# Performance work log

Hardware: AMD Instinct MI355X
Metric: run time of the kernel (lower is better)

## Reference

```python
import jax, jax.numpy as jnp
import numpy as np

GRAPH_SIZE = 1024
D_MODEL = 256
BATCH = 32
INITIAL_ALPHA = 1.0


def setup_inputs() -> dict:
    key = jax.random.key(0)
    ks = jax.random.split(key, 10)
    s = 1.0 / np.sqrt(D_MODEL)  # torch Linear default init scale
    inp = {
        "query": jax.random.normal(ks[0], (BATCH, GRAPH_SIZE, D_MODEL), jnp.float32),
        "key_": jax.random.normal(ks[1], (BATCH, GRAPH_SIZE, D_MODEL), jnp.float32),
        "value": jax.random.normal(ks[2], (BATCH, GRAPH_SIZE, D_MODEL), jnp.float32),
        "dist": jax.random.uniform(ks[3], (BATCH, GRAPH_SIZE, GRAPH_SIZE), jnp.float32),
        "Wq": jax.random.uniform(ks[4], (D_MODEL, D_MODEL), jnp.float32, -s, s),
        "bq": jax.random.uniform(ks[5], (D_MODEL,), jnp.float32, -s, s),
        "Wk": jax.random.uniform(ks[6], (D_MODEL, D_MODEL), jnp.float32, -s, s),
        "bk": jax.random.uniform(ks[7], (D_MODEL,), jnp.float32, -s, s),
        "Wv": jax.random.uniform(ks[8], (D_MODEL, D_MODEL), jnp.float32, -s, s),
        "bv": jax.random.uniform(ks[9], (D_MODEL,), jnp.float32, -s, s),
        # alpha_raw = exp(initial_alpha - 1)
        "alpha_raw": jnp.asarray(np.exp(INITIAL_ALPHA - 1.0), jnp.float32),
    }
    return inp


def reference(query, key_, value, dist, Wq, bq, Wk, bk, Wv, bv, alpha_raw):
    # self-attention path: mask=None, cross=False, query_size == graph_size
    log2_N = jnp.log2(jnp.asarray(GRAPH_SIZE, jnp.float32))
    alpha = jax.nn.softplus(alpha_raw) + 1e-6

    q = jnp.einsum('bnd,ed->bne', query, Wq) + bq   # fc_q
    k = jnp.einsum('bnd,ed->bne', key_, Wk) + bk    # fc_k
    v = jnp.einsum('bnd,ed->bne', value, Wv) + bv   # fc_v

    exp_A = jnp.exp(-alpha * log2_N * dist)         # [b, n, n]
    exp_K = jnp.exp(k)                              # [b, n, d]

    numerator = jnp.einsum('bqk,bkd->bqd', exp_A, exp_K * v)
    denominator = jnp.einsum('bqk,bkd->bqd', exp_A, exp_K) + 1e-8
    return jax.nn.sigmoid(q) * (numerator / denominator)
```

## Files before the change

### kernel.cpp

```cpp
#include <hip/hip_runtime.h>
#include <hip/hip_bf16.h>

#define NBATCH 32
#define NG 1024
#define DM 256

typedef short bf16x8 __attribute__((ext_vector_type(8)));
typedef float f32x4 __attribute__((ext_vector_type(4)));
typedef unsigned short u16x4 __attribute__((ext_vector_type(4)));
typedef unsigned short u16x8 __attribute__((ext_vector_type(8)));

static __device__ __forceinline__ unsigned short f2bf(float f) {
    __hip_bfloat16 h = __float2bfloat16(f);
    return *reinterpret_cast<unsigned short*>(&h);
}

static __device__ __forceinline__ void gload16(const void* g, void* l) {
    __builtin_amdgcn_global_load_lds(
        (const __attribute__((address_space(1))) unsigned int*)g,
        (__attribute__((address_space(3))) unsigned int*)l, 16, 0, 0);
}

static __device__ __forceinline__ void wait_vm8_bar() {
    asm volatile("s_waitcnt vmcnt(8)" ::: "memory");
    asm volatile("s_barrier" ::: "memory");
    __builtin_amdgcn_sched_barrier(0);
}
static __device__ __forceinline__ void wait_vm0_bar() {
    asm volatile("s_waitcnt vmcnt(0)" ::: "memory");
    asm volatile("s_barrier" ::: "memory");
    __builtin_amdgcn_sched_barrier(0);
}
static __device__ __forceinline__ void bar_only() {
    asm volatile("s_barrier" ::: "memory");
}

__global__ __launch_bounds__(256) void wpack_kernel(
    const float* __restrict__ Wq, const float* __restrict__ Wk,
    const float* __restrict__ Wv, unsigned short* __restrict__ Wb)
{
    const int i4 = (blockIdx.x * 256 + threadIdx.x) * 4;
    const int t = i4 >> 16;
    const int off = i4 & 65535;
    const float* src = (t == 0) ? Wq : (t == 1) ? Wk : Wv;
    float4 v = *(const float4*)(src + off);
    *(u16x4*)(Wb + i4) = (u16x4){ f2bf(v.x), f2bf(v.y), f2bf(v.z), f2bf(v.w) };
}

__global__ __launch_bounds__(256) void conv3_kernel(
    const float* __restrict__ q, const float* __restrict__ k,
    const float* __restrict__ v, unsigned short* __restrict__ Xb)
{
    const int sel = blockIdx.x >> 12;
    const float* src = (sel == 0) ? q : (sel == 1) ? k : v;
    const size_t i8 = (((size_t)(blockIdx.x & 4095)) * 256 + threadIdx.x) * 8;
    float4 a = *(const float4*)(src + i8);
    float4 b = *(const float4*)(src + i8 + 4);
    *(u16x8*)(Xb + (size_t)sel * NBATCH * NG * DM + i8) =
        (u16x8){ f2bf(a.x), f2bf(a.y), f2bf(a.z), f2bf(a.w),
                 f2bf(b.x), f2bf(b.y), f2bf(b.z), f2bf(b.w) };
}

__global__ __launch_bounds__(256) void exp_kernel(
    const float* __restrict__ dist, unsigned short* __restrict__ ea,
    const float* __restrict__ alpha_raw)
{
    const float alpha = log1pf(__expf(alpha_raw[0])) + 1e-6f;
    const float sc = -alpha * 10.0f * 1.44269504088896f;
    const size_t i8 = ((size_t)blockIdx.x * 256 + threadIdx.x) * 8;
    float4 v0 = *(const float4*)(dist + i8);
    float4 v1 = *(const float4*)(dist + i8 + 4);
    u16x8 o = { f2bf(exp2f(sc * v0.x)), f2bf(exp2f(sc * v0.y)),
                f2bf(exp2f(sc * v0.z)), f2bf(exp2f(sc * v0.w)),
                f2bf(exp2f(sc * v1.x)), f2bf(exp2f(sc * v1.y)),
                f2bf(exp2f(sc * v1.z)), f2bf(exp2f(sc * v1.w)) };
    *(u16x8*)(ea + i8) = o;
}

__global__ __launch_bounds__(256) void projq_kernel(
    const unsigned short* __restrict__ Xq,
    const unsigned short* __restrict__ Wb,
    const float* __restrict__ bq,
    float* __restrict__ sigq)
{
    __shared__ __align__(128) unsigned short lds[2][2][128 * 64];

    const int bid = blockIdx.x;
    const int mt = bid >> 1, nt = bid & 1;
    const int tid = threadIdx.x;
    const int w = tid >> 6, lane = tid & 63;
    const int wm = w >> 1, wn = w & 1;
    const int l15 = lane & 15, lhi = lane >> 4;
    const int lr = lane >> 3, sl = lane & 7;
    const int sp = sl ^ lr;

    const char* Abase = (const char*)(Xq + (size_t)mt * 128 * 256);
    const char* Wbase = (const char*)(Wb + (size_t)nt * 128 * 256);

    f32x4 acc[4][4];
    #pragma unroll
    for (int mi = 0; mi < 4; ++mi)
        #pragma unroll
        for (int ni = 0; ni < 4; ++ni)
            acc[mi][ni] = (f32x4){0.f, 0.f, 0.f, 0.f};

    auto STAGE = [&](int buf, int t) {
        #pragma unroll
        for (int i = 0; i < 4; ++i) {
            const int r = w * 32 + i * 8 + lr;
            gload16(Abase + (size_t)r * 512 + t * 128 + sp * 16,
                    (char*)&lds[buf][0][0] + w * 4096 + i * 1024);
            gload16(Wbase + (size_t)r * 512 + t * 128 + sp * 16,
                    (char*)&lds[buf][1][0] + w * 4096 + i * 1024);
        }
    };

    STAGE(0, 0);
    int cur = 0;
    for (int t = 0; t < 4; ++t) {
        if (t < 3) { STAGE(cur ^ 1, t + 1); wait_vm8_bar(); }
        else       { wait_vm0_bar(); }
        const char* Ab = (const char*)&lds[cur][0][0];
        const char* Bb = (const char*)&lds[cur][1][0];
        #pragma unroll
        for (int kk = 0; kk < 2; ++kk) {
            bf16x8 af[4], bfr[4];
            #pragma unroll
            for (int mi = 0; mi < 4; ++mi) {
                const int tr = wm * 64 + mi * 16 + l15;
                af[mi] = *(const bf16x8*)(Ab + ((tr * 128 + kk * 64 + lhi * 16) ^ ((tr & 7) << 4)));
            }
            #pragma unroll
            for (int ni = 0; ni < 4; ++ni) {
                const int tr = wn * 64 + ni * 16 + l15;
                bfr[ni] = *(const bf16x8*)(Bb + ((tr * 128 + kk * 64 + lhi * 16) ^ ((tr & 7) << 4)));
            }
            #pragma unroll
            for (int mi = 0; mi < 4; ++mi)
                #pragma unroll
                for (int ni = 0; ni < 4; ++ni)
                    acc[mi][ni] = __builtin_amdgcn_mfma_f32_16x16x32_bf16(
                        af[mi], bfr[ni], acc[mi][ni], 0, 0, 0);
        }
        bar_only();
        cur ^= 1;
    }

    #pragma unroll
    for (int ni = 0; ni < 4; ++ni) {
        const int c = nt * 128 + wn * 64 + ni * 16 + l15;
        const float bqs = bq[c];
        #pragma unroll
        for (int mi = 0; mi < 4; ++mi)
            #pragma unroll
            for (int r = 0; r < 4; ++r) {
                const size_t R = (size_t)mt * 128 + wm * 64 + mi * 16 + lhi * 4 + r;
                const float qv = acc[mi][ni][r] + bqs;
                sigq[R * DM + c] = 1.0f / (1.0f + __expf(-qv));
            }
    }
}

__global__ __launch_bounds__(256) void projkv_kernel(
    const unsigned short* __restrict__ Xk,
    const unsigned short* __restrict__ Xv,
    const unsigned short* __restrict__ Wkb,
    const unsigned short* __restrict__ Wvb,
    const float* __restrict__ bk, const float* __restrict__ bv,
    unsigned short* __restrict__ Pt)
{
    __shared__ __align__(128) unsigned short lds[2][2][128 * 64];

    const int bid = blockIdx.x;
    const int mt = bid >> 1, nt = bid & 1;
    const int tid = threadIdx.x;
    const int w = tid >> 6, lane = tid & 63;
    const int wm = w >> 1, wn = w & 1;
    const int l15 = lane & 15, lhi = lane >> 4;
    const int lr = lane >> 3, sl = lane & 7;
    const int sp = sl ^ lr;
    const int g16 = (sp & 3) * 16;

    f32x4 kacc[4][4], vacc[4][4];
    #pragma unroll
    for (int mi = 0; mi < 4; ++mi)
        #pragma unroll
        for (int ni = 0; ni < 4; ++ni) {
            kacc[mi][ni] = (f32x4){0.f, 0.f, 0.f, 0.f};
            vacc[mi][ni] = (f32x4){0.f, 0.f, 0.f, 0.f};
        }

    auto STAGE = [&](int buf, int t) {
        #pragma unroll
        for (int i = 0; i < 4; ++i) {
            const int r = w * 32 + i * 8 + lr;
            const char* asrc = (sp < 4 ? (const char*)Xk : (const char*)Xv)
                               + (size_t)(mt * 128 + r) * 512 + t * 64 + g16;
            gload16(asrc, (char*)&lds[buf][0][0] + w * 4096 + i * 1024);
            const char* wsrc = (sp < 4 ? (const char*)Wkb : (const char*)Wvb)
                               + (size_t)(nt * 128 + r) * 512 + t * 64 + g16;
            gload16(wsrc, (char*)&lds[buf][1][0] + w * 4096 + i * 1024);
        }
    };

    STAGE(0, 0);
    int cur = 0;
    for (int t = 0; t < 8; ++t) {
        if (t < 7) { STAGE(cur ^ 1, t + 1); wait_vm8_bar(); }
        else       { wait_vm0_bar(); }
        const char* Ab = (const char*)&lds[cur][0][0];
        const char* Bb = (const char*)&lds[cur][1][0];
        bf16x8 kaf[4], vaf[4], kbf[4], vbf[4];
        #pragma unroll
        for (int mi = 0; mi < 4; ++mi) {
            const int tr = wm * 64 + mi * 16 + l15;
            const int sw = (tr & 7) << 4;
            kaf[mi] = *(const bf16x8*)(Ab + ((tr * 128 + lhi * 16) ^ sw));
            vaf[mi] = *(const bf16x8*)(Ab + ((tr * 128 + 64 + lhi * 16) ^ sw));
        }
        #pragma unroll
        for (int ni = 0; ni < 4; ++ni) {
            const int tr = wn * 64 + ni * 16 + l15;
            const int sw = (tr & 7) << 4;
            kbf[ni] = *(const bf16x8*)(Bb + ((tr * 128 + lhi * 16) ^ sw));
            vbf[ni] = *(const bf16x8*)(Bb + ((tr * 128 + 64 + lhi * 16) ^ sw));
        }
        #pragma unroll
        for (int mi = 0; mi < 4; ++mi)
            #pragma unroll
            for (int ni = 0; ni < 4; ++ni) {
                kacc[mi][ni] = __builtin_amdgcn_mfma_f32_16x16x32_bf16(
                    kaf[mi], kbf[ni], kacc[mi][ni], 0, 0, 0);
                vacc[mi][ni] = __builtin_amdgcn_mfma_f32_16x16x32_bf16(
                    vaf[mi], vbf[ni], vacc[mi][ni], 0, 0, 0);
            }
        bar_only();
        cur ^= 1;
    }

    const int b = (mt * 128) >> 10;
    const int kb0 = (mt * 128) & 1023;
    #pragma unroll
    for (int ni = 0; ni < 4; ++ni) {
        const int c = nt * 128 + wn * 64 + ni * 16 + l15;
        const float bks = bk[c], bvs = bv[c];
        #pragma unroll
        for (int mi = 0; mi < 4; ++mi) {
            unsigned short p1[4], p2[4];
            #pragma unroll
            for (int r = 0; r < 4; ++r) {
                const float ek = __expf(kacc[mi][ni][r] + bks);
                const float vv = vacc[mi][ni][r] + bvs;
                p1[r] = f2bf(ek * vv);
                p2[r] = f2bf(ek);
            }
            const int kidx = kb0 + wm * 64 + mi * 16 + lhi * 4;
            *(u16x4*)&Pt[((size_t)b * 512 + 2 * c    ) * NG + kidx] =
                (u16x4){p1[0], p1[1], p1[2], p1[3]};
            *(u16x4*)&Pt[((size_t)b * 512 + 2 * c + 1) * NG + kidx] =
                (u16x4){p2[0], p2[1], p2[2], p2[3]};
        }
    }
}

__global__ __launch_bounds__(256) void attn_kernel(
    const unsigned short* __restrict__ ea,
    const unsigned short* __restrict__ Pt,
    float* __restrict__ out)
{
    __shared__ __align__(128) unsigned short lds[2][2][128 * 64];

    const int bid = blockIdx.x;
    const int l = (bid & 7) * 128 + (bid >> 3);
    const int b = l >> 5;
    const int m = (l >> 2) & 7;
    const int n = l & 3;

    const int tid = threadIdx.x;
    const int w = tid >> 6, lane = tid & 63;
    const int wm = w >> 1, wn = w & 1;
    const int l15 = lane & 15, lhi = lane >> 4;
    const int lr = lane >> 3, cb = lane & 7;
    const int cbs = cb ^ lr;

    const char* Abase = (const char*)(ea + ((size_t)b * NG + m * 128) * NG);
    const char* Bbase = (const char*)(Pt + ((size_t)b * 512 + n * 128) * NG);

    f32x4 acc[4][4];
    #pragma unroll
    for (int mi = 0; mi < 4; ++mi)
        #pragma unroll
        for (int ni = 0; ni < 4; ++ni)
            acc[mi][ni] = (f32x4){0.f, 0.f, 0.f, 0.f};

    auto STAGE = [&](int buf, int t) {
        #pragma unroll
        for (int i = 0; i < 4; ++i) {
            const int r = w * 32 + i * 8 + lr;
            const size_t goff = (size_t)r * 2048 + t * 128 + cbs * 16;
            char* ldst = (char*)&lds[buf][0][0] + w * 4096 + i * 1024;
            gload16(Abase + goff, ldst);
            gload16(Bbase + goff, ldst + 16384);
        }
    };

    STAGE(0, 0);
    int cur = 0;
    for (int t = 0; t < 16; ++t) {
        if (t < 15) { STAGE(cur ^ 1, t + 1); wait_vm8_bar(); }
        else        { wait_vm0_bar(); }
        const char* Ab = (const char*)&lds[cur][0][0];
        const char* Bb = (const char*)&lds[cur][1][0];
        #pragma unroll
        for (int kk = 0; kk < 2; ++kk) {
            const int bc = kk * 64 + lhi * 16;
            bf16x8 af[4], bfr[4];
            #pragma unroll
            for (int mi = 0; mi < 4; ++mi) {
                const int tr = wm * 64 + mi * 16 + l15;
                af[mi] = *(const bf16x8*)(Ab + ((tr * 128 + bc) ^ ((tr & 7) << 4)));
            }
            #pragma unroll
            for (int ni = 0; ni < 4; ++ni) {
                const int tr = wn * 64 + ni * 16 + l15;
                bfr[ni] = *(const bf16x8*)(Bb + ((tr * 128 + bc) ^ ((tr & 7) << 4)));
            }
            #pragma unroll
            for (int mi = 0; mi < 4; ++mi)
                #pragma unroll
                for (int ni = 0; ni < 4; ++ni)
                    acc[mi][ni] = __builtin_amdgcn_mfma_f32_16x16x32_bf16(
                        af[mi], bfr[ni], acc[mi][ni], 0, 0, 0);
        }
        bar_only();
        cur ^= 1;
    }

    const int parity = lane & 1;
    #pragma unroll
    for (int mi = 0; mi < 4; ++mi)
        #pragma unroll
        for (int ni = 0; ni < 4; ++ni)
            #pragma unroll
            for (int r = 0; r < 4; ++r) {
                const float own = acc[mi][ni][r];
                const float other = __shfl_xor(own, 1, 64);
                if (!parity) {
                    const int colg = n * 128 + wn * 64 + ni * 16 + l15;
                    const int d = colg >> 1;
                    const int rowg = m * 128 + wm * 64 + mi * 16 + lhi * 4 + r;
                    const size_t idx = ((size_t)b * NG + rowg) * DM + d;
                    out[idx] = out[idx] * (own / (other + 1e-8f));
                }
            }
}

extern "C" void kernel_launch(void* const* d_in, const int* in_sizes, int n_in,
                              void* d_out, int out_size, void* d_ws, size_t ws_size,
                              hipStream_t stream) {
    const float* query = (const float*)d_in[0];
    const float* key_  = (const float*)d_in[1];
    const float* value = (const float*)d_in[2];
    const float* dist  = (const float*)d_in[3];
    const float* Wq = (const float*)d_in[4];
    const float* bq = (const float*)d_in[5];
    const float* Wk = (const float*)d_in[6];
    const float* bk = (const float*)d_in[7];
    const float* Wv = (const float*)d_in[8];
    const float* bv = (const float*)d_in[9];
    const float* alpha_raw = (const float*)d_in[10];
    float* out = (float*)d_out;

    unsigned short* Pt = (unsigned short*)d_ws;
    unsigned short* ea = Pt + (size_t)NBATCH * 512 * NG;
    unsigned short* Xb = ea + (size_t)NBATCH * NG * NG;
    const size_t XN = (size_t)NBATCH * NG * DM;
    unsigned short* Wb = Xb + 3 * XN;

    wpack_kernel<<<dim3(192), dim3(256), 0, stream>>>(Wq, Wk, Wv, Wb);
    conv3_kernel<<<dim3(12288), dim3(256), 0, stream>>>(query, key_, value, Xb);

    projq_kernel<<<dim3(512), dim3(256), 0, stream>>>(Xb, Wb, bq, out);
    projkv_kernel<<<dim3(512), dim3(256), 0, stream>>>(
        Xb + XN, Xb + 2 * XN, Wb + 65536, Wb + 131072, bk, bv, Pt);

    exp_kernel<<<dim3(16384), dim3(256), 0, stream>>>(dist, ea, alpha_raw);
    attn_kernel<<<dim3(1024), dim3(256), 0, stream>>>(ea, Pt, out);
}
```

Measured before the change: 195.3 us.

## Enlarge attention GEMM tile to 256x256 with 8 warps and K-step 32

The attention GEMM moves from 128x128 output tiles with 4 warps to 256x256 tiles with 8 warps, so each of 256 blocks covers four times the output area. Half the warps stage A and half stage B, and the K chunk per stage shrinks to 32 with 32 iterations. The XOR swizzle on LDS is dropped. The aim is to raise data reuse and cut global/L2 traffic for the ea and Pt operands. The cost is more registers per thread, fewer blocks (256 on a large GPU), possible LDS bank conflicts without the swizzle, and more barriers per unit of work.

```diff
diff --git a/kernel.cpp b/kernel.cpp
--- a/kernel.cpp
+++ b/kernel.cpp
@@ -23,6 +23,11 @@
 
 static __device__ __forceinline__ void wait_vm8_bar() {
     asm volatile("s_waitcnt vmcnt(8)" ::: "memory");
+    asm volatile("s_barrier" ::: "memory");
+    __builtin_amdgcn_sched_barrier(0);
+}
+static __device__ __forceinline__ void wait_vm4_bar() {
+    asm volatile("s_waitcnt vmcnt(4)" ::: "memory");
     asm volatile("s_barrier" ::: "memory");
     __builtin_amdgcn_sched_barrier(0);
 }
@@ -263,32 +268,36 @@
     }
 }
 
-__global__ __launch_bounds__(256) void attn_kernel(
+__global__ __launch_bounds__(512, 2) void attn_kernel(
     const unsigned short* __restrict__ ea,
     const unsigned short* __restrict__ Pt,
     float* __restrict__ out)
 {
-    __shared__ __align__(128) unsigned short lds[2][2][128 * 64];
+    __shared__ __align__(128) char lds[2][2][16384];
 
     const int bid = blockIdx.x;
-    const int l = (bid & 7) * 128 + (bid >> 3);
-    const int b = l >> 5;
-    const int m = (l >> 2) & 7;
-    const int n = l & 3;
+    const int l = (bid & 7) * 32 + (bid >> 3);
+    const int b = l >> 3;
+    const int m = (l >> 1) & 3;
+    const int n = l & 1;
 
     const int tid = threadIdx.x;
     const int w = tid >> 6, lane = tid & 63;
-    const int wm = w >> 1, wn = w & 1;
+    const int wm = w >> 2, wn = w & 3;
     const int l15 = lane & 15, lhi = lane >> 4;
-    const int lr = lane >> 3, cb = lane & 7;
-    const int cbs = cb ^ lr;
-
-    const char* Abase = (const char*)(ea + ((size_t)b * NG + m * 128) * NG);
-    const char* Bbase = (const char*)(Pt + ((size_t)b * 512 + n * 128) * NG);
-
-    f32x4 acc[4][4];
-    #pragma unroll
-    for (int mi = 0; mi < 4; ++mi)
+
+    const int isB = w >> 2;
+    const int sw = w & 3;
+    const int srow = lane >> 2;
+    const int sg = lane & 3;
+
+    const char* Abase = (const char*)(ea + ((size_t)b * NG + m * 256) * NG);
+    const char* Bbase = (const char*)(Pt + ((size_t)b * 512 + n * 256) * NG);
+    const char* Sbase = isB ? Bbase : Abase;
+
+    f32x4 acc[8][4];
+    #pragma unroll
+    for (int mi = 0; mi < 8; ++mi)
         #pragma unroll
         for (int ni = 0; ni < 4; ++ni)
             acc[mi][ni] = (f32x4){0.f, 0.f, 0.f, 0.f};
@@ -296,49 +305,43 @@
     auto STAGE = [&](int buf, int t) {
         #pragma unroll
         for (int i = 0; i < 4; ++i) {
-            const int r = w * 32 + i * 8 + lr;
-            const size_t goff = (size_t)r * 2048 + t * 128 + cbs * 16;
-            char* ldst = (char*)&lds[buf][0][0] + w * 4096 + i * 1024;
-            gload16(Abase + goff, ldst);
-            gload16(Bbase + goff, ldst + 16384);
+            const int r = sw * 64 + i * 16 + srow;
+            gload16(Sbase + (size_t)r * 2048 + t * 64 + sg * 16,
+                    &lds[buf][isB][0] + sw * 4096 + i * 1024);
         }
     };
 
     STAGE(0, 0);
     int cur = 0;
-    for (int t = 0; t < 16; ++t) {
-        if (t < 15) { STAGE(cur ^ 1, t + 1); wait_vm8_bar(); }
+    for (int t = 0; t < 32; ++t) {
+        if (t < 31) { STAGE(cur ^ 1, t + 1); wait_vm4_bar(); }
         else        { wait_vm0_bar(); }
-        const char* Ab = (const char*)&lds[cur][0][0];
-        const char* Bb = (const char*)&lds[cur][1][0];
-        #pragma unroll
-        for (int kk = 0; kk < 2; ++kk) {
-            const int bc = kk * 64 + lhi * 16;
-            bf16x8 af[4], bfr[4];
-            #pragma unroll
-            for (int mi = 0; mi < 4; ++mi) {
-                const int tr = wm * 64 + mi * 16 + l15;
-                af[mi] = *(const bf16x8*)(Ab + ((tr * 128 + bc) ^ ((tr & 7) << 4)));
-            }
-            #pragma unroll
-            for (int ni = 0; ni < 4; ++ni) {
-                const int tr = wn * 64 + ni * 16 + l15;
-                bfr[ni] = *(const bf16x8*)(Bb + ((tr * 128 + bc) ^ ((tr & 7) << 4)));
-            }
-            #pragma unroll
-            for (int mi = 0; mi < 4; ++mi)
-                #pragma unroll
-                for (int ni = 0; ni < 4; ++ni)
-                    acc[mi][ni] = __builtin_amdgcn_mfma_f32_16x16x32_bf16(
-                        af[mi], bfr[ni], acc[mi][ni], 0, 0, 0);
-        }
+        const char* Ab = &lds[cur][0][0];
+        const char* Bb = &lds[cur][1][0];
+        bf16x8 af[8], bfr[4];
+        #pragma unroll
+        for (int mi = 0; mi < 8; ++mi) {
+            const int tr = wm * 128 + mi * 16 + l15;
+            af[mi] = *(const bf16x8*)(Ab + tr * 64 + lhi * 16);
+        }
+        #pragma unroll
+        for (int ni = 0; ni < 4; ++ni) {
+            const int tr = wn * 64 + ni * 16 + l15;
+            bfr[ni] = *(const bf16x8*)(Bb + tr * 64 + lhi * 16);
+        }
+        #pragma unroll
+        for (int mi = 0; mi < 8; ++mi)
+            #pragma unroll
+            for (int ni = 0; ni < 4; ++ni)
+                acc[mi][ni] = __builtin_amdgcn_mfma_f32_16x16x32_bf16(
+                    af[mi], bfr[ni], acc[mi][ni], 0, 0, 0);
         bar_only();
         cur ^= 1;
     }
 
     const int parity = lane & 1;
     #pragma unroll
-    for (int mi = 0; mi < 4; ++mi)
+    for (int mi = 0; mi < 8; ++mi)
         #pragma unroll
         for (int ni = 0; ni < 4; ++ni)
             #pragma unroll
@@ -346,9 +349,9 @@
                 const float own = acc[mi][ni][r];
                 const float other = __shfl_xor(own, 1, 64);
                 if (!parity) {
-                    const int colg = n * 128 + wn * 64 + ni * 16 + l15;
+                    const int colg = n * 256 + wn * 64 + ni * 16 + l15;
                     const int d = colg >> 1;
-                    const int rowg = m * 128 + wm * 64 + mi * 16 + lhi * 4 + r;
+                    const int rowg = m * 256 + wm * 128 + mi * 16 + lhi * 4 + r;
                     const size_t idx = ((size_t)b * NG + rowg) * DM + d;
                     out[idx] = out[idx] * (own / (other + 1e-8f));
                 }
@@ -385,5 +388,5 @@
         Xb + XN, Xb + 2 * XN, Wb + 65536, Wb + 131072, bk, bv, Pt);
 
     exp_kernel<<<dim3(16384), dim3(256), 0, stream>>>(dist, ea, alpha_raw);
-    attn_kernel<<<dim3(1024), dim3(256), 0, stream>>>(ea, Pt, out);
-}
+    attn_kernel<<<dim3(256), dim3(512), 0, stream>>>(ea, Pt, out);
+}
```

Measured after the change: 182.4 us. -6.6%, faster.
